# Kernel tuning notes

Measured on AMD Instinct MI355X. Metric: run time of the kernel, lower is better.

The kernel has to match this reference:

```python
import jax, jax.numpy as jnp
import numpy as np
import math

D_MODEL = 1024
NUM_HEADS = 16
D_K = D_MODEL // NUM_HEADS
NUM_BUCKETS = 32
MAX_DISTANCE = 512  # PositionalEncoding max_len


def _relative_position_bucket(relative_position):
    # Faithful to the torch code: both signs add num_buckets//2 (==16), rp==0 adds 0.
    half = NUM_BUCKETS // 2            # 16
    max_exact = NUM_BUCKETS // 4       # 8
    base = (relative_position > 0).astype(jnp.int32) * half \
         + (relative_position < 0).astype(jnp.int32) * half
    arp = jnp.abs(relative_position)
    is_small = arp < max_exact
    safe = jnp.maximum(arp, 1).astype(jnp.float32)  # avoid log(0); masked by is_small anyway
    large = max_exact + (jnp.log(safe / max_exact)
                         / math.log(MAX_DISTANCE / max_exact)
                         * (half - max_exact)).astype(jnp.int32)  # trunc == torch .long()
    large = jnp.minimum(large, half - 1)
    return base + jnp.where(is_small, arp, large)


def compute_bias(rel_bias_table, seq_length):
    ctx = jnp.arange(seq_length, dtype=jnp.int32)[:, None]
    mem = jnp.arange(seq_length, dtype=jnp.int32)[None, :]
    buckets = _relative_position_bucket(mem - ctx)        # [S, S]
    values = rel_bias_table[buckets]                       # [S, S, H]
    return jnp.transpose(values, (2, 0, 1))[None]          # [1, H, S, S]


def setup_inputs() -> dict:
    key = jax.random.key(0)
    ks = jax.random.split(key, 12)
    B, S, D = 2, 2048, D_MODEL
    scale = 1.0 / math.sqrt(D)
    inp = {
        "query": jax.random.normal(ks[0], (B, S, D), jnp.float32),
        "key": jax.random.normal(ks[1], (B, S, D), jnp.float32),
        "value": jax.random.normal(ks[2], (B, S, D), jnp.float32),
        "Wq": jax.random.normal(ks[3], (D, D), jnp.float32) * scale,
        "bq": jnp.zeros((D,), jnp.float32),
        "Wk": jax.random.normal(ks[4], (D, D), jnp.float32) * scale,
        "bk": jnp.zeros((D,), jnp.float32),
        "Wv": jax.random.normal(ks[5], (D, D), jnp.float32) * scale,
        "bv": jnp.zeros((D,), jnp.float32),
        "Wo": jax.random.normal(ks[6], (D, D), jnp.float32) * scale,
        "bo": jnp.zeros((D,), jnp.float32),
        "rel_bias_table": jax.random.normal(ks[7], (NUM_BUCKETS, NUM_HEADS), jnp.float32) * 0.1,
    }
    return inp


def reference(query, key, value, Wq, bq, Wk, bk, Wv, bv, Wo, bo, rel_bias_table):
    B, Sq, D = query.shape
    Sk = key.shape[1]
    H, dk = NUM_HEADS, D_K
    q = (query @ Wq + bq).reshape(B, Sq, H, dk)
    k = (key @ Wk + bk).reshape(B, Sk, H, dk)
    v = (value @ Wv + bv).reshape(B, Sk, H, dk)
    scores = jnp.einsum('bqhd,bkhd->bhqk', q, k) / math.sqrt(dk)  # [B,H,Sq,Sk]
    position_bias = compute_bias(rel_bias_table, max(Sq, Sk))[:, :, :Sq, :Sk]
    scores = scores + position_bias  # broadcast over batch (torch expand)
    attn_weights = jax.nn.softmax(scores, axis=-1)
    # dropout is identity in eval / p=0
    context = jnp.einsum('bhqk,bkhd->bqhd', attn_weights, v).reshape(B, Sq, D)
    output = context @ Wo + bo
    pb = jnp.broadcast_to(position_bias, (B, H, Sq, Sk))
    return output, attn_weights, pb
```

## Files before the change

kernel.cpp:

```cpp
#include <hip/hip_runtime.h>
#include <hip/hip_bf16.h>

#define BN 2
#define SEQ 2048
#define DM 1024
#define NH 16
#define DK 64

using f32x4  = __attribute__((ext_vector_type(4))) float;
using bf16x8 = __attribute__((ext_vector_type(8))) __bf16;
using short8 = __attribute__((ext_vector_type(8))) short;

static_assert(sizeof(bf16x8) == 16, "bf16x8 must be 16B");

#define MFMA16(a, b, c) __builtin_amdgcn_mfma_f32_16x16x32_bf16(a, b, c, 0, 0, 0)

__device__ __forceinline__ unsigned short f2b(float f) {
    __hip_bfloat16 h = __float2bfloat16(f);
    return __builtin_bit_cast(unsigned short, h);
}

__device__ __forceinline__ bf16x8 load_bf8(const unsigned short* p) {
    short8 s = *reinterpret_cast<const short8*>(p);
    return __builtin_bit_cast(bf16x8, s);
}

__global__ void bias_table_kernel(const float* __restrict__ rel,
                                  float* __restrict__ bias_val) {
    int idx = blockIdx.x * 256 + threadIdx.x;
    if (idx >= NH * 4095) return;
    int h = idx / 4095;
    int dd = idx - h * 4095;
    int d = dd - 2047;
    int a = d < 0 ? -d : d;
    int bucket;
    if (a == 0) bucket = 0;
    else if (a < 8) bucket = 16 + a;
    else {
        int k = (a >= 14) + (a >= 23) + (a >= 39) + (a >= 64) +
                (a >= 108) + (a >= 182) + (a >= 305);
        bucket = 24 + k;
    }
    bias_val[h * 4095 + dd] = rel[bucket * NH + h];
}

template<int AMODE, int OMODE>
__global__ __launch_bounds__(256) void proj_gemm(const void* __restrict__ Ain,
        const float* __restrict__ W, const float* __restrict__ bias,
        void* __restrict__ Out, float outscale) {
    constexpr int KP = 40;
    __shared__ unsigned short la[128 * KP];
    __shared__ unsigned short lb[128 * KP];
    const int tid = threadIdx.x;
    const int bx = blockIdx.x & 7, by = blockIdx.x >> 3;
    const int m0 = by * 128, n0 = bx * 128;
    const int lane = tid & 63, wid = tid >> 6;
    const int wm0 = (wid >> 1) * 64, wn0 = (wid & 1) * 64;
    const int l15 = lane & 15, l4 = lane >> 4;
    f32x4 acc[4][4] = {};

    for (int kt = 0; kt < 32; ++kt) {
        const int k0 = kt * 32;
        if (AMODE == 0) {
            const float* A = (const float*)Ain;
#pragma unroll
            for (int i = 0; i < 4; ++i) {
                int idx = tid + i * 256;
                int row = idx >> 3, c4 = (idx & 7) * 4;
                float4 v = *(const float4*)(A + (size_t)(m0 + row) * DM + k0 + c4);
                ushort4 u; u.x = f2b(v.x); u.y = f2b(v.y); u.z = f2b(v.z); u.w = f2b(v.w);
                *(ushort4*)&la[row * KP + c4] = u;
            }
        } else {
            const unsigned short* A = (const unsigned short*)Ain;
#pragma unroll
            for (int i = 0; i < 2; ++i) {
                int idx = tid + i * 256;
                int row = idx >> 2, c8 = (idx & 3) * 8;
                int4 v = *(const int4*)(A + (size_t)(m0 + row) * DM + k0 + c8);
                *(int4*)&la[row * KP + c8] = v;
            }
        }
#pragma unroll
        for (int i = 0; i < 4; ++i) {
            int idx = tid + i * 256;
            int n = idx & 127, k4 = (idx >> 7) * 4;
            const float* wp = W + (size_t)(k0 + k4) * DM + n0 + n;
            ushort4 u;
            u.x = f2b(wp[0 * DM]); u.y = f2b(wp[1 * DM]);
            u.z = f2b(wp[2 * DM]); u.w = f2b(wp[3 * DM]);
            *(ushort4*)&lb[n * KP + k4] = u;
        }
        __syncthreads();
        bf16x8 af[4], bfv[4];
#pragma unroll
        for (int m = 0; m < 4; ++m)
            af[m] = load_bf8(&la[(wm0 + m * 16 + l15) * KP + l4 * 8]);
#pragma unroll
        for (int n = 0; n < 4; ++n)
            bfv[n] = load_bf8(&lb[(wn0 + n * 16 + l15) * KP + l4 * 8]);
#pragma unroll
        for (int m = 0; m < 4; ++m)
#pragma unroll
            for (int n = 0; n < 4; ++n)
                acc[m][n] = MFMA16(af[m], bfv[n], acc[m][n]);
        __syncthreads();
    }

    float bv[4];
#pragma unroll
    for (int n = 0; n < 4; ++n) bv[n] = bias[n0 + wn0 + n * 16 + l15];
#pragma unroll
    for (int m = 0; m < 4; ++m) {
#pragma unroll
        for (int n = 0; n < 4; ++n) {
            int gcol = n0 + wn0 + n * 16 + l15;
#pragma unroll
            for (int r = 0; r < 4; ++r) {
                int grow = m0 + wm0 + m * 16 + l4 * 4 + r;
                float val = (acc[m][n][r] + bv[n]) * outscale;
                if (OMODE == 0) {
                    ((unsigned short*)Out)[(size_t)grow * DM + gcol] = f2b(val);
                } else if (OMODE == 1) {
                    int b = grow >> 11, s = grow & 2047;
                    int hh = gcol >> 6, dl = gcol & 63;
                    ((unsigned short*)Out)[(((size_t)(b * NH + hh) * DK + dl) << 11) + s] = f2b(val);
                } else {
                    ((float*)Out)[(size_t)grow * DM + gcol] = val;
                }
            }
        }
    }
}

__global__ __launch_bounds__(256) void attn2_kernel(
        const unsigned short* __restrict__ Qp, const unsigned short* __restrict__ Kp,
        const unsigned short* __restrict__ Vt, const float* __restrict__ bias_val,
        float* __restrict__ attn_out, unsigned short* __restrict__ ctx) {
    __shared__ float bias_lds[2112];
    __shared__ float wtile[4][16 * 36];
    const int tid = threadIdx.x;
    const int lane = tid & 63, wid = tid >> 6;
    const int l15 = lane & 15, l4 = lane >> 4;
    const int bid = (blockIdx.x & 7) * 128 + (blockIdx.x >> 3);
    const int qb = bid & 31;
    const int h = (bid >> 5) & 15;
    const int b = bid >> 9;
    const int q0 = qb * 64;
    const int qw = q0 + wid * 16;

    {
        const float* bp = bias_val + h * 4095 + (2047 - (q0 + 63));
        for (int i = tid; i < 2111; i += 256) bias_lds[i] = bp[i];
    }
    __syncthreads();

    const unsigned short* qbase = Qp + (size_t)(b * SEQ + qw + l15) * DM + h * DK;
    bf16x8 qa0 = load_bf8(qbase + l4 * 8);
    bf16x8 qa1 = load_bf8(qbase + 32 + l4 * 8);

    const unsigned short* kbase = Kp + (size_t)b * SEQ * DM + h * DK;
    const int bbase = 63 - wid * 16 - l4 * 4;

    float m[4], l[4];
#pragma unroll
    for (int r = 0; r < 4; ++r) { m[r] = -3e38f; l[r] = 0.f; }

    for (int c0 = 0; c0 < SEQ; c0 += 32) {
        const unsigned short* kp = kbase + (size_t)(c0 + l15) * DM;
        bf16x8 k00 = load_bf8(kp + l4 * 8);
        bf16x8 k01 = load_bf8(kp + 32 + l4 * 8);
        bf16x8 k10 = load_bf8(kp + 16 * DM + l4 * 8);
        bf16x8 k11 = load_bf8(kp + 16 * DM + 32 + l4 * 8);
        f32x4 a0 = {}, a1 = {};
        a0 = MFMA16(qa0, k00, a0); a0 = MFMA16(qa1, k01, a0);
        a1 = MFMA16(qa0, k10, a1); a1 = MFMA16(qa1, k11, a1);
#pragma unroll
        for (int r = 0; r < 4; ++r) {
            float s0 = a0[r] + bias_lds[c0 + l15 + bbase - r];
            float s1 = a1[r] + bias_lds[c0 + 16 + l15 + bbase - r];
            float cm = fmaxf(s0, s1);
            if (cm > m[r]) { l[r] *= __expf(m[r] - cm); m[r] = cm; }
            l[r] += __expf(s0 - m[r]) + __expf(s1 - m[r]);
        }
    }
#pragma unroll
    for (int off = 1; off < 16; off <<= 1) {
#pragma unroll
        for (int r = 0; r < 4; ++r) {
            float om = __shfl_xor(m[r], off);
            float ol = __shfl_xor(l[r], off);
            float M = fmaxf(m[r], om);
            l[r] = l[r] * __expf(m[r] - M) + ol * __expf(om - M);
            m[r] = M;
        }
    }
    float invl[4];
#pragma unroll
    for (int r = 0; r < 4; ++r) invl[r] = 1.0f / l[r];

    float* wt = wtile[wid];
    float* abase = attn_out + ((size_t)((b * NH + h) * SEQ + qw)) * SEQ;
    const unsigned short* vbase = Vt + (((size_t)(b * NH + h) * DK) << 11);
    f32x4 cacc[4] = {};

    bf16x8 k00, k01, k10, k11;
    {
        const unsigned short* kp = kbase + (size_t)l15 * DM;
        k00 = load_bf8(kp + l4 * 8);
        k01 = load_bf8(kp + 32 + l4 * 8);
        k10 = load_bf8(kp + 16 * DM + l4 * 8);
        k11 = load_bf8(kp + 16 * DM + 32 + l4 * 8);
    }
    for (int c0 = 0; c0 < SEQ; c0 += 32) {
        f32x4 a0 = {}, a1 = {};
        a0 = MFMA16(qa0, k00, a0); a0 = MFMA16(qa1, k01, a0);
        a1 = MFMA16(qa0, k10, a1); a1 = MFMA16(qa1, k11, a1);
        const int cn = (c0 + 32) & (SEQ - 1);
        const unsigned short* kp = kbase + (size_t)(cn + l15) * DM;
        k00 = load_bf8(kp + l4 * 8);
        k01 = load_bf8(kp + 32 + l4 * 8);
        k10 = load_bf8(kp + 16 * DM + l4 * 8);
        k11 = load_bf8(kp + 16 * DM + 32 + l4 * 8);
        bf16x8 vv0 = load_bf8(vbase + ((size_t)(0 * 16 + l15) << 11) + c0 + l4 * 8);
        bf16x8 vv1 = load_bf8(vbase + ((size_t)(1 * 16 + l15) << 11) + c0 + l4 * 8);
        bf16x8 vv2 = load_bf8(vbase + ((size_t)(2 * 16 + l15) << 11) + c0 + l4 * 8);
        bf16x8 vv3 = load_bf8(vbase + ((size_t)(3 * 16 + l15) << 11) + c0 + l4 * 8);
#pragma unroll
        for (int r = 0; r < 4; ++r) {
            int row = l4 * 4 + r;
            float w0 = __expf(a0[r] + bias_lds[c0 + l15 + bbase - r] - m[r]) * invl[r];
            float w1 = __expf(a1[r] + bias_lds[c0 + 16 + l15 + bbase - r] - m[r]) * invl[r];
            wt[row * 36 + l15] = w0;
            wt[row * 36 + 16 + l15] = w1;
        }
        asm volatile("s_waitcnt lgkmcnt(0)" ::: "memory");
        __builtin_amdgcn_sched_barrier(0);
        {
            int row = lane >> 2, cg = (lane & 3) * 8;
            float4 v0 = *(const float4*)&wt[row * 36 + cg];
            float4 v1 = *(const float4*)&wt[row * 36 + cg + 4];
            float* gp = abase + (size_t)row * SEQ + c0 + cg;
            *(float4*)gp = v0;
            *(float4*)(gp + 4) = v1;
        }
        float4 pA = *(const float4*)&wt[l15 * 36 + l4 * 8];
        float4 pB = *(const float4*)&wt[l15 * 36 + l4 * 8 + 4];
        short8 ps;
        ps[0] = (short)f2b(pA.x); ps[1] = (short)f2b(pA.y);
        ps[2] = (short)f2b(pA.z); ps[3] = (short)f2b(pA.w);
        ps[4] = (short)f2b(pB.x); ps[5] = (short)f2b(pB.y);
        ps[6] = (short)f2b(pB.z); ps[7] = (short)f2b(pB.w);
        bf16x8 pf = __builtin_bit_cast(bf16x8, ps);
        cacc[0] = MFMA16(pf, vv0, cacc[0]);
        cacc[1] = MFMA16(pf, vv1, cacc[1]);
        cacc[2] = MFMA16(pf, vv2, cacc[2]);
        cacc[3] = MFMA16(pf, vv3, cacc[3]);
        asm volatile("s_waitcnt lgkmcnt(0)" ::: "memory");
        __builtin_amdgcn_sched_barrier(0);
    }
#pragma unroll
    for (int d0 = 0; d0 < 4; ++d0)
#pragma unroll
        for (int r = 0; r < 4; ++r)
            ctx[(size_t)(b * SEQ + qw + l4 * 4 + r) * DM + h * DK + d0 * 16 + l15] =
                f2b(cacc[d0][r]);
}

__global__ __launch_bounds__(256) void pb_kernel(const float* __restrict__ bias_val,
                                                 float* __restrict__ pb) {
    unsigned int t4 = blockIdx.x * 256u + threadIdx.x;
    int j = (t4 & 511) * 4;
    int i = (t4 >> 9) & 2047;
    int h = t4 >> 20;
    const float* bp = bias_val + h * 4095 + (j - i + 2047);
    float4 v; v.x = bp[0]; v.y = bp[1]; v.z = bp[2]; v.w = bp[3];
    size_t off = ((size_t)(h * SEQ + i) << 11) + j;
    *(float4*)(pb + off) = v;
    *(float4*)(pb + off + (size_t)NH * SEQ * SEQ) = v;
}

extern "C" void kernel_launch(void* const* d_in, const int* in_sizes, int n_in,
                              void* d_out, int out_size, void* d_ws, size_t ws_size,
                              hipStream_t stream) {
    const float* query = (const float*)d_in[0];
    const float* key   = (const float*)d_in[1];
    const float* value = (const float*)d_in[2];
    const float* Wq = (const float*)d_in[3];
    const float* bq = (const float*)d_in[4];
    const float* Wk = (const float*)d_in[5];
    const float* bk = (const float*)d_in[6];
    const float* Wv = (const float*)d_in[7];
    const float* bv = (const float*)d_in[8];
    const float* Wo = (const float*)d_in[9];
    const float* bo = (const float*)d_in[10];
    const float* rel = (const float*)d_in[11];

    float* out = (float*)d_out;
    float* attn_out = out + (size_t)BN * SEQ * DM;
    float* pb_out = attn_out + (size_t)BN * NH * SEQ * SEQ;

    char* ws = (char*)d_ws;
    float* bias_val = (float*)ws;
    unsigned short* Qp = (unsigned short*)(ws + 262144);
    unsigned short* Kp = Qp + (size_t)BN * SEQ * DM;
    unsigned short* Vt = Kp + (size_t)BN * SEQ * DM;
    unsigned short* ctx = Vt + (size_t)BN * SEQ * DM;

    bias_table_kernel<<<256, 256, 0, stream>>>(rel, bias_val);
    proj_gemm<0, 0><<<256, 256, 0, stream>>>(query, Wq, bq, Qp, 0.125f);
    proj_gemm<0, 0><<<256, 256, 0, stream>>>(key, Wk, bk, Kp, 1.0f);
    proj_gemm<0, 1><<<256, 256, 0, stream>>>(value, Wv, bv, Vt, 1.0f);
    attn2_kernel<<<BN * NH * (SEQ / 64), 256, 0, stream>>>(Qp, Kp, Vt, bias_val, attn_out, ctx);
    proj_gemm<1, 2><<<256, 256, 0, stream>>>(ctx, Wo, bo, out, 1.0f);
    pb_kernel<<<65536, 256, 0, stream>>>(bias_val, pb_out);
}
```

Baseline: 710.0 us.

## Pre-transpose weights, batch QKV GEMMs, head-major K, fuse position-bias writes into attention

Adds a kernel that converts all four weight matrices to transposed bf16 once, so the GEMMs load B tiles with wide contiguous loads instead of strided scalar float loads. The three QKV projections become one launch over a z-dimension, K is stored head-major for contiguous per-head reads, and the output projection uses a smaller 64-row tile to get more blocks. The separate position-bias broadcast kernel is removed; the attention kernel now writes position_bias rows from its LDS bias copy alongside the attention weights. This trades an extra transpose pass and more workspace for fewer launches and better memory access, and the attention kernel now carries the extra pb store traffic.

Result: faster. 601.0 us (-15.3%).

```diff
diff --git a/kernel.cpp b/kernel.cpp
--- a/kernel.cpp
+++ b/kernel.cpp
@@ -44,16 +44,60 @@
     bias_val[h * 4095 + dd] = rel[bucket * NH + h];
 }
 
-template<int AMODE, int OMODE>
-__global__ __launch_bounds__(256) void proj_gemm(const void* __restrict__ Ain,
-        const float* __restrict__ W, const float* __restrict__ bias,
-        void* __restrict__ Out, float outscale) {
+__global__ __launch_bounds__(256) void wtrans_kernel(
+        const float* __restrict__ W0, const float* __restrict__ W1,
+        const float* __restrict__ W2, const float* __restrict__ W3,
+        unsigned short* __restrict__ T0, unsigned short* __restrict__ T1,
+        unsigned short* __restrict__ T2, unsigned short* __restrict__ T3) {
+    constexpr int P = 68;
+    __shared__ unsigned short lt[64 * P];
+    const int mz = blockIdx.z;
+    const float* W = mz == 0 ? W0 : mz == 1 ? W1 : mz == 2 ? W2 : W3;
+    unsigned short* T = mz == 0 ? T0 : mz == 1 ? T1 : mz == 2 ? T2 : T3;
+    const int k0 = blockIdx.x * 64, n0 = blockIdx.y * 64;
+    const int tid = threadIdx.x;
+#pragma unroll
+    for (int p = 0; p < 4; ++p) {
+        int r = p * 16 + (tid >> 4);
+        int c = (tid & 15) * 4;
+        float4 vv = *(const float4*)&W[(size_t)(k0 + r) * DM + n0 + c];
+#pragma unroll
+        for (int j = 0; j < 4; ++j) {
+            int n = c + j;
+            float x = j == 0 ? vv.x : j == 1 ? vv.y : j == 2 ? vv.z : vv.w;
+            lt[n * P + (r ^ ((n & 7) << 3))] = f2b(x);
+        }
+    }
+    __syncthreads();
+#pragma unroll
+    for (int p = 0; p < 2; ++p) {
+        int rn = p * 32 + (tid >> 3);
+        int ck = (tid & 7) * 8;
+        int ckx = ck ^ ((rn & 7) << 3);
+        ushort4 a0 = *(ushort4*)&lt[rn * P + ckx];
+        ushort4 a1 = *(ushort4*)&lt[rn * P + ckx + 4];
+        *(ushort4*)&T[(size_t)(n0 + rn) * DM + k0 + ck] = a0;
+        *(ushort4*)&T[(size_t)(n0 + rn) * DM + k0 + ck + 4] = a1;
+    }
+}
+
+__global__ __launch_bounds__(256) void qkv_gemm(
+        const float* __restrict__ Aq, const float* __restrict__ Ak, const float* __restrict__ Av,
+        const unsigned short* __restrict__ Wtq, const unsigned short* __restrict__ Wtk,
+        const unsigned short* __restrict__ Wtv,
+        const float* __restrict__ bq, const float* __restrict__ bk, const float* __restrict__ bv,
+        unsigned short* __restrict__ Qp, unsigned short* __restrict__ Kh,
+        unsigned short* __restrict__ Vt) {
     constexpr int KP = 40;
     __shared__ unsigned short la[128 * KP];
     __shared__ unsigned short lb[128 * KP];
+    const int mat = blockIdx.z;
+    const float* A = mat == 0 ? Aq : mat == 1 ? Ak : Av;
+    const unsigned short* Wt = mat == 0 ? Wtq : mat == 1 ? Wtk : Wtv;
+    const float* bias = mat == 0 ? bq : mat == 1 ? bk : bv;
+    const float outscale = mat == 0 ? 0.125f : 1.0f;
     const int tid = threadIdx.x;
-    const int bx = blockIdx.x & 7, by = blockIdx.x >> 3;
-    const int m0 = by * 128, n0 = bx * 128;
+    const int m0 = blockIdx.y * 128, n0 = blockIdx.x * 128;
     const int lane = tid & 63, wid = tid >> 6;
     const int wm0 = (wid >> 1) * 64, wn0 = (wid & 1) * 64;
     const int l15 = lane & 15, l4 = lane >> 4;
@@ -61,35 +105,20 @@
 
     for (int kt = 0; kt < 32; ++kt) {
         const int k0 = kt * 32;
-        if (AMODE == 0) {
-            const float* A = (const float*)Ain;
-#pragma unroll
-            for (int i = 0; i < 4; ++i) {
-                int idx = tid + i * 256;
-                int row = idx >> 3, c4 = (idx & 7) * 4;
-                float4 v = *(const float4*)(A + (size_t)(m0 + row) * DM + k0 + c4);
-                ushort4 u; u.x = f2b(v.x); u.y = f2b(v.y); u.z = f2b(v.z); u.w = f2b(v.w);
-                *(ushort4*)&la[row * KP + c4] = u;
-            }
-        } else {
-            const unsigned short* A = (const unsigned short*)Ain;
-#pragma unroll
-            for (int i = 0; i < 2; ++i) {
-                int idx = tid + i * 256;
-                int row = idx >> 2, c8 = (idx & 3) * 8;
-                int4 v = *(const int4*)(A + (size_t)(m0 + row) * DM + k0 + c8);
-                *(int4*)&la[row * KP + c8] = v;
-            }
-        }
 #pragma unroll
         for (int i = 0; i < 4; ++i) {
             int idx = tid + i * 256;
-            int n = idx & 127, k4 = (idx >> 7) * 4;
-            const float* wp = W + (size_t)(k0 + k4) * DM + n0 + n;
-            ushort4 u;
-            u.x = f2b(wp[0 * DM]); u.y = f2b(wp[1 * DM]);
-            u.z = f2b(wp[2 * DM]); u.w = f2b(wp[3 * DM]);
-            *(ushort4*)&lb[n * KP + k4] = u;
+            int row = idx >> 3, c4 = (idx & 7) * 4;
+            float4 v = *(const float4*)(A + (size_t)(m0 + row) * DM + k0 + c4);
+            ushort4 u; u.x = f2b(v.x); u.y = f2b(v.y); u.z = f2b(v.z); u.w = f2b(v.w);
+            *(ushort4*)&la[row * KP + c4] = u;
+        }
+#pragma unroll
+        for (int i = 0; i < 2; ++i) {
+            int idx = tid + i * 256;
+            int row = idx >> 2, c8 = (idx & 3) * 8;
+            *(int4*)&lb[row * KP + c8] =
+                *(const int4*)&Wt[(size_t)(n0 + row) * DM + k0 + c8];
         }
         __syncthreads();
         bf16x8 af[4], bfv[4];
@@ -107,9 +136,9 @@
         __syncthreads();
     }
 
-    float bv[4];
-#pragma unroll
-    for (int n = 0; n < 4; ++n) bv[n] = bias[n0 + wn0 + n * 16 + l15];
+    float bv4[4];
+#pragma unroll
+    for (int n = 0; n < 4; ++n) bv4[n] = bias[n0 + wn0 + n * 16 + l15];
 #pragma unroll
     for (int m = 0; m < 4; ++m) {
 #pragma unroll
@@ -118,25 +147,84 @@
 #pragma unroll
             for (int r = 0; r < 4; ++r) {
                 int grow = m0 + wm0 + m * 16 + l4 * 4 + r;
-                float val = (acc[m][n][r] + bv[n]) * outscale;
-                if (OMODE == 0) {
-                    ((unsigned short*)Out)[(size_t)grow * DM + gcol] = f2b(val);
-                } else if (OMODE == 1) {
-                    int b = grow >> 11, s = grow & 2047;
-                    int hh = gcol >> 6, dl = gcol & 63;
-                    ((unsigned short*)Out)[(((size_t)(b * NH + hh) * DK + dl) << 11) + s] = f2b(val);
+                float val = (acc[m][n][r] + bv4[n]) * outscale;
+                unsigned short ob = f2b(val);
+                int b = grow >> 11, s = grow & 2047;
+                int hh = gcol >> 6, dl = gcol & 63;
+                if (mat == 0) {
+                    Qp[(size_t)grow * DM + gcol] = ob;
+                } else if (mat == 1) {
+                    Kh[(((size_t)(b * NH + hh) * SEQ + s) << 6) + dl] = ob;
                 } else {
-                    ((float*)Out)[(size_t)grow * DM + gcol] = val;
+                    Vt[(((size_t)(b * NH + hh) * DK + dl) << 11) + s] = ob;
                 }
             }
         }
     }
 }
 
-__global__ __launch_bounds__(256) void attn2_kernel(
-        const unsigned short* __restrict__ Qp, const unsigned short* __restrict__ Kp,
+__global__ __launch_bounds__(256) void o_gemm(
+        const unsigned short* __restrict__ Actx, const unsigned short* __restrict__ Wto,
+        const float* __restrict__ bo, float* __restrict__ out) {
+    constexpr int KP = 40;
+    __shared__ unsigned short la[64 * KP];
+    __shared__ unsigned short lb[128 * KP];
+    const int tid = threadIdx.x;
+    const int m0 = blockIdx.y * 64, n0 = blockIdx.x * 128;
+    const int lane = tid & 63, wid = tid >> 6;
+    const int wm0 = (wid >> 1) * 32, wn0 = (wid & 1) * 64;
+    const int l15 = lane & 15, l4 = lane >> 4;
+    f32x4 acc[2][4] = {};
+
+    for (int kt = 0; kt < 32; ++kt) {
+        const int k0 = kt * 32;
+        {
+            int row = tid >> 2, c8 = (tid & 3) * 8;
+            *(int4*)&la[row * KP + c8] =
+                *(const int4*)&Actx[(size_t)(m0 + row) * DM + k0 + c8];
+        }
+#pragma unroll
+        for (int i = 0; i < 2; ++i) {
+            int idx = tid + i * 256;
+            int row = idx >> 2, c8 = (idx & 3) * 8;
+            *(int4*)&lb[row * KP + c8] =
+                *(const int4*)&Wto[(size_t)(n0 + row) * DM + k0 + c8];
+        }
+        __syncthreads();
+        bf16x8 af[2], bfv[4];
+#pragma unroll
+        for (int m = 0; m < 2; ++m)
+            af[m] = load_bf8(&la[(wm0 + m * 16 + l15) * KP + l4 * 8]);
+#pragma unroll
+        for (int n = 0; n < 4; ++n)
+            bfv[n] = load_bf8(&lb[(wn0 + n * 16 + l15) * KP + l4 * 8]);
+#pragma unroll
+        for (int m = 0; m < 2; ++m)
+#pragma unroll
+            for (int n = 0; n < 4; ++n)
+                acc[m][n] = MFMA16(af[m], bfv[n], acc[m][n]);
+        __syncthreads();
+    }
+
+#pragma unroll
+    for (int m = 0; m < 2; ++m)
+#pragma unroll
+        for (int n = 0; n < 4; ++n) {
+            int gcol = n0 + wn0 + n * 16 + l15;
+            float bb = bo[gcol];
+#pragma unroll
+            for (int r = 0; r < 4; ++r) {
+                int grow = m0 + wm0 + m * 16 + l4 * 4 + r;
+                out[(size_t)grow * DM + gcol] = acc[m][n][r] + bb;
+            }
+        }
+}
+
+__global__ __launch_bounds__(256) void attn3_kernel(
+        const unsigned short* __restrict__ Qp, const unsigned short* __restrict__ Kh,
         const unsigned short* __restrict__ Vt, const float* __restrict__ bias_val,
-        float* __restrict__ attn_out, unsigned short* __restrict__ ctx) {
+        float* __restrict__ attn_out, float* __restrict__ pb_out,
+        unsigned short* __restrict__ ctx) {
     __shared__ float bias_lds[2112];
     __shared__ float wtile[4][16 * 36];
     const int tid = threadIdx.x;
@@ -159,7 +247,7 @@
     bf16x8 qa0 = load_bf8(qbase + l4 * 8);
     bf16x8 qa1 = load_bf8(qbase + 32 + l4 * 8);
 
-    const unsigned short* kbase = Kp + (size_t)b * SEQ * DM + h * DK;
+    const unsigned short* kbase = Kh + (((size_t)(b * NH + h) * SEQ) << 6);
     const int bbase = 63 - wid * 16 - l4 * 4;
 
     float m[4], l[4];
@@ -167,11 +255,11 @@
     for (int r = 0; r < 4; ++r) { m[r] = -3e38f; l[r] = 0.f; }
 
     for (int c0 = 0; c0 < SEQ; c0 += 32) {
-        const unsigned short* kp = kbase + (size_t)(c0 + l15) * DM;
+        const unsigned short* kp = kbase + ((size_t)(c0 + l15) << 6);
         bf16x8 k00 = load_bf8(kp + l4 * 8);
         bf16x8 k01 = load_bf8(kp + 32 + l4 * 8);
-        bf16x8 k10 = load_bf8(kp + 16 * DM + l4 * 8);
-        bf16x8 k11 = load_bf8(kp + 16 * DM + 32 + l4 * 8);
+        bf16x8 k10 = load_bf8(kp + (16 << 6) + l4 * 8);
+        bf16x8 k11 = load_bf8(kp + (16 << 6) + 32 + l4 * 8);
         f32x4 a0 = {}, a1 = {};
         a0 = MFMA16(qa0, k00, a0); a0 = MFMA16(qa1, k01, a0);
         a1 = MFMA16(qa0, k10, a1); a1 = MFMA16(qa1, k11, a1);
@@ -201,27 +289,29 @@
 
     float* wt = wtile[wid];
     float* abase = attn_out + ((size_t)((b * NH + h) * SEQ + qw)) * SEQ;
+    float* pbase = pb_out + ((size_t)((b * NH + h) * SEQ + qw)) * SEQ;
     const unsigned short* vbase = Vt + (((size_t)(b * NH + h) * DK) << 11);
     f32x4 cacc[4] = {};
 
     bf16x8 k00, k01, k10, k11;
     {
-        const unsigned short* kp = kbase + (size_t)l15 * DM;
+        const unsigned short* kp = kbase + ((size_t)l15 << 6);
         k00 = load_bf8(kp + l4 * 8);
         k01 = load_bf8(kp + 32 + l4 * 8);
-        k10 = load_bf8(kp + 16 * DM + l4 * 8);
-        k11 = load_bf8(kp + 16 * DM + 32 + l4 * 8);
-    }
+        k10 = load_bf8(kp + (16 << 6) + l4 * 8);
+        k11 = load_bf8(kp + (16 << 6) + 32 + l4 * 8);
+    }
+    const int srow = lane >> 2, scg = (lane & 3) * 8;
     for (int c0 = 0; c0 < SEQ; c0 += 32) {
         f32x4 a0 = {}, a1 = {};
         a0 = MFMA16(qa0, k00, a0); a0 = MFMA16(qa1, k01, a0);
         a1 = MFMA16(qa0, k10, a1); a1 = MFMA16(qa1, k11, a1);
         const int cn = (c0 + 32) & (SEQ - 1);
-        const unsigned short* kp = kbase + (size_t)(cn + l15) * DM;
+        const unsigned short* kp = kbase + ((size_t)(cn + l15) << 6);
         k00 = load_bf8(kp + l4 * 8);
         k01 = load_bf8(kp + 32 + l4 * 8);
-        k10 = load_bf8(kp + 16 * DM + l4 * 8);
-        k11 = load_bf8(kp + 16 * DM + 32 + l4 * 8);
+        k10 = load_bf8(kp + (16 << 6) + l4 * 8);
+        k11 = load_bf8(kp + (16 << 6) + 32 + l4 * 8);
         bf16x8 vv0 = load_bf8(vbase + ((size_t)(0 * 16 + l15) << 11) + c0 + l4 * 8);
         bf16x8 vv1 = load_bf8(vbase + ((size_t)(1 * 16 + l15) << 11) + c0 + l4 * 8);
         bf16x8 vv2 = load_bf8(vbase + ((size_t)(2 * 16 + l15) << 11) + c0 + l4 * 8);
@@ -237,12 +327,22 @@
         asm volatile("s_waitcnt lgkmcnt(0)" ::: "memory");
         __builtin_amdgcn_sched_barrier(0);
         {
-            int row = lane >> 2, cg = (lane & 3) * 8;
-            float4 v0 = *(const float4*)&wt[row * 36 + cg];
-            float4 v1 = *(const float4*)&wt[row * 36 + cg + 4];
-            float* gp = abase + (size_t)row * SEQ + c0 + cg;
+            float4 v0 = *(const float4*)&wt[srow * 36 + scg];
+            float4 v1 = *(const float4*)&wt[srow * 36 + scg + 4];
+            float* gp = abase + (size_t)srow * SEQ + c0 + scg;
             *(float4*)gp = v0;
             *(float4*)(gp + 4) = v1;
+        }
+        {
+            const int ib = c0 + scg + bbase + l4 * 4 - srow;
+            float4 p0, p1;
+            p0.x = bias_lds[ib + 0]; p0.y = bias_lds[ib + 1];
+            p0.z = bias_lds[ib + 2]; p0.w = bias_lds[ib + 3];
+            p1.x = bias_lds[ib + 4]; p1.y = bias_lds[ib + 5];
+            p1.z = bias_lds[ib + 6]; p1.w = bias_lds[ib + 7];
+            float* gp = pbase + (size_t)srow * SEQ + c0 + scg;
+            *(float4*)gp = p0;
+            *(float4*)(gp + 4) = p1;
         }
         float4 pA = *(const float4*)&wt[l15 * 36 + l4 * 8];
         float4 pB = *(const float4*)&wt[l15 * 36 + l4 * 8 + 4];
@@ -265,19 +365,6 @@
         for (int r = 0; r < 4; ++r)
             ctx[(size_t)(b * SEQ + qw + l4 * 4 + r) * DM + h * DK + d0 * 16 + l15] =
                 f2b(cacc[d0][r]);
-}
-
-__global__ __launch_bounds__(256) void pb_kernel(const float* __restrict__ bias_val,
-                                                 float* __restrict__ pb) {
-    unsigned int t4 = blockIdx.x * 256u + threadIdx.x;
-    int j = (t4 & 511) * 4;
-    int i = (t4 >> 9) & 2047;
-    int h = t4 >> 20;
-    const float* bp = bias_val + h * 4095 + (j - i + 2047);
-    float4 v; v.x = bp[0]; v.y = bp[1]; v.z = bp[2]; v.w = bp[3];
-    size_t off = ((size_t)(h * SEQ + i) << 11) + j;
-    *(float4*)(pb + off) = v;
-    *(float4*)(pb + off + (size_t)NH * SEQ * SEQ) = v;
 }
 
 extern "C" void kernel_launch(void* const* d_in, const int* in_sizes, int n_in,
@@ -302,16 +389,20 @@
 
     char* ws = (char*)d_ws;
     float* bias_val = (float*)ws;
-    unsigned short* Qp = (unsigned short*)(ws + 262144);
-    unsigned short* Kp = Qp + (size_t)BN * SEQ * DM;
-    unsigned short* Vt = Kp + (size_t)BN * SEQ * DM;
+    unsigned short* Qp  = (unsigned short*)(ws + 262144);
+    unsigned short* Kh  = Qp + (size_t)BN * SEQ * DM;
+    unsigned short* Vt  = Kh + (size_t)BN * SEQ * DM;
     unsigned short* ctx = Vt + (size_t)BN * SEQ * DM;
+    unsigned short* Wtq = ctx + (size_t)BN * SEQ * DM;
+    unsigned short* Wtk = Wtq + (size_t)DM * DM;
+    unsigned short* Wtv = Wtk + (size_t)DM * DM;
+    unsigned short* Wto = Wtv + (size_t)DM * DM;
 
     bias_table_kernel<<<256, 256, 0, stream>>>(rel, bias_val);
-    proj_gemm<0, 0><<<256, 256, 0, stream>>>(query, Wq, bq, Qp, 0.125f);
-    proj_gemm<0, 0><<<256, 256, 0, stream>>>(key, Wk, bk, Kp, 1.0f);
-    proj_gemm<0, 1><<<256, 256, 0, stream>>>(value, Wv, bv, Vt, 1.0f);
-    attn2_kernel<<<BN * NH * (SEQ / 64), 256, 0, stream>>>(Qp, Kp, Vt, bias_val, attn_out, ctx);
-    proj_gemm<1, 2><<<256, 256, 0, stream>>>(ctx, Wo, bo, out, 1.0f);
-    pb_kernel<<<65536, 256, 0, stream>>>(bias_val, pb_out);
-}
+    wtrans_kernel<<<dim3(16, 16, 4), 256, 0, stream>>>(Wq, Wk, Wv, Wo, Wtq, Wtk, Wtv, Wto);
+    qkv_gemm<<<dim3(8, 32, 3), 256, 0, stream>>>(query, key, value, Wtq, Wtk, Wtv,
+                                                 bq, bk, bv, Qp, Kh, Vt);
+    attn3_kernel<<<BN * NH * (SEQ / 64), 256, 0, stream>>>(Qp, Kh, Vt, bias_val,
+                                                           attn_out, pb_out, ctx);
+    o_gemm<<<dim3(8, 64), 256, 0, stream>>>(ctx, Wto, bo, out);
+}
```
